# Optimization experiments

Measured on AMD Instinct MI355X. Metric: run time of the kernel, lower is better.

Reference implementation:

```python
import jax, jax.numpy as jnp
import numpy as np

RC = 6.0  # cosine cutoff radius

def _cut_fn(r):
    # Behler cosine cutoff: 0.5*(cos(pi*r/rc)+1) for r < rc, else 0
    return jnp.where(r < RC, 0.5 * (jnp.cos(jnp.pi * r / RC) + 1.0), 0.0)

def setup_inputs() -> dict:
    key = jax.random.key(0)
    ks = jax.random.split(key, 6)
    B, N, T, E, Z = 4, 256, 512, 16, 4
    def dist(k):
        return jax.random.uniform(k, (B, N, T), dtype=jnp.float32) * 5.0 + 0.5
    r_ij = dist(ks[0])
    r_ik = dist(ks[1])
    r_jk = dist(ks[2])
    # binary triple mask (float, as multiplied in the original forward)
    mask_triples = (jax.random.uniform(ks[3], (B, N, T)) > 0.3).astype(jnp.float32)
    etas = jax.random.uniform(ks[4], (E,), dtype=jnp.float32) + 0.5
    zetas = jnp.array([1.0, 2.0, 4.0, 8.0], dtype=jnp.float32)
    return {"r_ij": r_ij, "r_ik": r_ik, "r_jk": r_jk,
            "mask_triples": mask_triples, "etas": etas, "zetas": zetas}

def reference(r_ij, r_ik, r_jk, mask_triples, etas, zetas):
    # r_ij, r_ik, r_jk, mask_triples: (B, N, T); etas: (E,); zetas: (Z,)
    r2 = r_ij ** 2 + r_ik ** 2 + r_jk ** 2                       # (B,N,T)
    cut = _cut_fn(r_ij) * _cut_fn(r_ik) * _cut_fn(r_jk)          # (B,N,T)
    radius_part = jnp.exp(-r2[..., None] * etas) * cut[..., None]  # (B,N,T,E)
    cos_theta = r2 / (2.0 * r_ij * r_ik)                          # (B,N,T)
    cos_theta = jnp.where(mask_triples == 0, 0.0, cos_theta)
    base = (1.0 - cos_theta)[..., None] ** zetas                  # (B,N,T,Z)
    angular_part = jnp.concatenate(
        [2.0 ** (1.0 - zetas) * base, 2.0 ** (1.0 + zetas) * base], axis=-1
    )                                                             # (B,N,T,2Z)
    # fused masked outer-product + sum over triples dim (dim 2 in the original)
    f = jnp.einsum('bnt,bnte,bntz->bnez', mask_triples, radius_part, angular_part)
    B, N = r_ij.shape[:2]
    return f.reshape(B, N, -1)                                    # (B,N,E*2Z)
```

## Files before the change

kernel.cpp:

```cpp
#include <hip/hip_runtime.h>
#include <math.h>


#define T_TRIP 512
#define E_N 16

__global__ __launch_bounds__(256) void behler_g2_kernel(
    const float* __restrict__ r_ij, const float* __restrict__ r_ik,
    const float* __restrict__ r_jk, const float* __restrict__ mask,
    const float* __restrict__ etas, const float* __restrict__ zetas,
    float* __restrict__ out)
{
    __shared__ float  R2[T_TRIP];
    __shared__ float4 P[T_TRIP];
    __shared__ float  red[4][E_N][4];

    const int blk = blockIdx.x;
    const int tid = threadIdx.x;
    const size_t b2 = (size_t)blk * (T_TRIP / 2) + tid;

    const float z0 = zetas[0], z1 = zetas[1], z2 = zetas[2], z3 = zetas[3];
    const bool fastz = (z0 == 1.0f && z1 == 2.0f && z2 == 4.0f && z3 == 8.0f);
    const float PI_OVER_RC = 0.52359877559829887f;

    const float2 va = ((const float2*)r_ij)[b2];
    const float2 vb = ((const float2*)r_ik)[b2];
    const float2 vc = ((const float2*)r_jk)[b2];
    const float2 vm = ((const float2*)mask)[b2];

    float r2s[2];
    float4 ps[2];
    #pragma unroll
    for (int k = 0; k < 2; ++k) {
        float a = k ? va.y : va.x;
        float b = k ? vb.y : vb.x;
        float c = k ? vc.y : vc.x;
        float m = k ? vm.y : vm.x;
        float r2 = fmaf(a, a, fmaf(b, b, c * c));
        float fa  = (a < 6.0f) ? 0.5f * (__cosf(a * PI_OVER_RC) + 1.0f) : 0.0f;
        float fb  = (b < 6.0f) ? 0.5f * (__cosf(b * PI_OVER_RC) + 1.0f) : 0.0f;
        float fcv = (c < 6.0f) ? 0.5f * (__cosf(c * PI_OVER_RC) + 1.0f) : 0.0f;
        float w = m * fa * fb * fcv;
        float ct = __fdividef(r2, 2.0f * a * b);
        float4 p;
        if (fastz) {
            float bs = 1.0f - ct;
            float b2v = bs * bs, b4 = b2v * b2v, b8 = b4 * b4;
            p = make_float4(w * bs, w * b2v, w * b4, w * b8);
        } else {
            if (m == 0.0f) ct = 0.0f;
            float bs = 1.0f - ct;
            p = make_float4(w * powf(bs, z0), w * powf(bs, z1),
                            w * powf(bs, z2), w * powf(bs, z3));
        }
        r2s[k] = r2;
        ps[k] = p;
    }
    ((float2*)R2)[tid] = make_float2(r2s[0], r2s[1]);
    P[2 * tid]     = ps[0];
    P[2 * tid + 1] = ps[1];
    __syncthreads();

    const int g = tid >> 4;
    const int e = tid & 15;
    const float me = -etas[e];

    float acc0 = 0.0f, acc1 = 0.0f, acc2 = 0.0f, acc3 = 0.0f;
    #pragma unroll
    for (int i = 0; i < T_TRIP / 16; ++i) {
        int t = (i << 4) + g;
        float x = __expf(R2[t] * me);
        float4 p = P[t];
        acc0 = fmaf(x, p.x, acc0);
        acc1 = fmaf(x, p.y, acc1);
        acc2 = fmaf(x, p.z, acc2);
        acc3 = fmaf(x, p.w, acc3);
    }

    acc0 += __shfl_down(acc0, 32); acc0 += __shfl_down(acc0, 16);
    acc1 += __shfl_down(acc1, 32); acc1 += __shfl_down(acc1, 16);
    acc2 += __shfl_down(acc2, 32); acc2 += __shfl_down(acc2, 16);
    acc3 += __shfl_down(acc3, 32); acc3 += __shfl_down(acc3, 16);

    const int wave = tid >> 6;
    if ((tid & 63) < 16) {
        red[wave][e][0] = acc0;
        red[wave][e][1] = acc1;
        red[wave][e][2] = acc2;
        red[wave][e][3] = acc3;
    }
    __syncthreads();

    if (tid < 128) {
        int ee = tid >> 3, z = tid & 7, j = z & 3;
        float s = red[0][ee][j] + red[1][ee][j] + red[2][ee][j] + red[3][ee][j];
        float zj = zetas[j];
        float coef = exp2f((z < 4) ? (1.0f - zj) : (1.0f + zj));
        out[(size_t)blk * 128 + tid] = coef * s;
    }
}

extern "C" void kernel_launch(void* const* d_in, const int* in_sizes, int n_in,
                              void* d_out, int out_size, void* d_ws, size_t ws_size,
                              hipStream_t stream) {
    const float* r_ij = (const float*)d_in[0];
    const float* r_ik = (const float*)d_in[1];
    const float* r_jk = (const float*)d_in[2];
    const float* mask = (const float*)d_in[3];
    const float* etas = (const float*)d_in[4];
    const float* zetas = (const float*)d_in[5];
    float* out = (float*)d_out;

    int nblk = out_size / 128;
    behler_g2_kernel<<<nblk, 256, 0, stream>>>(r_ij, r_ik, r_jk, mask,
                                               etas, zetas, out);
}
```

Measured before the change: 9.734 us.

## Pack r2/base/log-weight in shared memory and fold weight into exp2

Instead of storing a float4 of weighted angular powers per triple, each triple now stores r2, the angular base and log2 of its cutoff weight in a repacked shared layout. In the main loop the weight is folded into the exponent via exp2(r2*eta*log2e + log2 w), and the zeta powers are recomputed by squaring in the inner loop. This reduces LDS traffic per triple at the cost of extra multiplies per (e, triple). A zero weight now relies on log2(0) giving -inf so that exp2 returns zero.

```diff
diff --git a/kernel.cpp b/kernel.cpp
--- a/kernel.cpp
+++ b/kernel.cpp
@@ -3,6 +3,7 @@
 
 
 #define T_TRIP 512
+#define NPAIR  (T_TRIP / 2)
 #define E_N 16
 
 __global__ __launch_bounds__(256) void behler_g2_kernel(
@@ -11,8 +12,8 @@
     const float* __restrict__ etas, const float* __restrict__ zetas,
     float* __restrict__ out)
 {
-    __shared__ float  R2[T_TRIP];
-    __shared__ float4 P[T_TRIP];
+    __shared__ float4 RB[NPAIR];
+    __shared__ float2 LW[NPAIR];
     __shared__ float  red[4][E_N][4];
 
     const int blk = blockIdx.x;
@@ -22,16 +23,16 @@
     const float z0 = zetas[0], z1 = zetas[1], z2 = zetas[2], z3 = zetas[3];
     const bool fastz = (z0 == 1.0f && z1 == 2.0f && z2 == 4.0f && z3 == 8.0f);
     const float PI_OVER_RC = 0.52359877559829887f;
+    const float LOG2E      = 1.4426950408889634f;
 
     const float2 va = ((const float2*)r_ij)[b2];
     const float2 vb = ((const float2*)r_ik)[b2];
     const float2 vc = ((const float2*)r_jk)[b2];
     const float2 vm = ((const float2*)mask)[b2];
 
-    float r2s[2];
-    float4 ps[2];
     #pragma unroll
     for (int k = 0; k < 2; ++k) {
+        int t = 2 * tid + k;
         float a = k ? va.y : va.x;
         float b = k ? vb.y : vb.x;
         float c = k ? vc.y : vc.x;
@@ -42,39 +43,52 @@
         float fcv = (c < 6.0f) ? 0.5f * (__cosf(c * PI_OVER_RC) + 1.0f) : 0.0f;
         float w = m * fa * fb * fcv;
         float ct = __fdividef(r2, 2.0f * a * b);
-        float4 p;
-        if (fastz) {
-            float bs = 1.0f - ct;
-            float b2v = bs * bs, b4 = b2v * b2v, b8 = b4 * b4;
-            p = make_float4(w * bs, w * b2v, w * b4, w * b8);
-        } else {
-            if (m == 0.0f) ct = 0.0f;
-            float bs = 1.0f - ct;
-            p = make_float4(w * powf(bs, z0), w * powf(bs, z1),
-                            w * powf(bs, z2), w * powf(bs, z3));
-        }
-        r2s[k] = r2;
-        ps[k] = p;
+        float bs = 1.0f - ct;
+        if (!fastz && m == 0.0f) bs = 0.0f;
+        float lw = __log2f(w);
+
+        int p    = (t >> 5) * 16 + (t & 15);
+        int slot = (t >> 4) & 1;
+        ((float2*)&RB[p])[slot] = make_float2(r2, bs);
+        ((float*)&LW[p])[slot]  = lw;
     }
-    ((float2*)R2)[tid] = make_float2(r2s[0], r2s[1]);
-    P[2 * tid]     = ps[0];
-    P[2 * tid + 1] = ps[1];
     __syncthreads();
 
     const int g = tid >> 4;
     const int e = tid & 15;
-    const float me = -etas[e];
+    const float me = -etas[e] * LOG2E;
 
     float acc0 = 0.0f, acc1 = 0.0f, acc2 = 0.0f, acc3 = 0.0f;
-    #pragma unroll
-    for (int i = 0; i < T_TRIP / 16; ++i) {
-        int t = (i << 4) + g;
-        float x = __expf(R2[t] * me);
-        float4 p = P[t];
-        acc0 = fmaf(x, p.x, acc0);
-        acc1 = fmaf(x, p.y, acc1);
-        acc2 = fmaf(x, p.z, acc2);
-        acc3 = fmaf(x, p.w, acc3);
+    if (fastz) {
+        #pragma unroll
+        for (int i = 0; i < NPAIR / 16; ++i) {
+            float4 rb = RB[i * 16 + g];
+            float2 lw = LW[i * 16 + g];
+            float xa = exp2f(fmaf(rb.x, me, lw.x));
+            float xb = exp2f(fmaf(rb.z, me, lw.y));
+            float s1 = rb.y, s2 = s1 * s1, s4 = s2 * s2, s8 = s4 * s4;
+            acc0 = fmaf(xa, s1, acc0);
+            acc1 = fmaf(xa, s2, acc1);
+            acc2 = fmaf(xa, s4, acc2);
+            acc3 = fmaf(xa, s8, acc3);
+            float u1 = rb.w, u2 = u1 * u1, u4 = u2 * u2, u8 = u4 * u4;
+            acc0 = fmaf(xb, u1, acc0);
+            acc1 = fmaf(xb, u2, acc1);
+            acc2 = fmaf(xb, u4, acc2);
+            acc3 = fmaf(xb, u8, acc3);
+        }
+    } else {
+        #pragma unroll 1
+        for (int i = 0; i < NPAIR / 16; ++i) {
+            float4 rb = RB[i * 16 + g];
+            float2 lw = LW[i * 16 + g];
+            float xa = exp2f(fmaf(rb.x, me, lw.x));
+            float xb = exp2f(fmaf(rb.z, me, lw.y));
+            acc0 = fmaf(xa, powf(rb.y, z0), acc0) + xb * powf(rb.w, z0);
+            acc1 = fmaf(xa, powf(rb.y, z1), acc1) + xb * powf(rb.w, z1);
+            acc2 = fmaf(xa, powf(rb.y, z2), acc2) + xb * powf(rb.w, z2);
+            acc3 = fmaf(xa, powf(rb.y, z3), acc3) + xb * powf(rb.w, z3);
+        }
     }
 
     acc0 += __shfl_down(acc0, 32); acc0 += __shfl_down(acc0, 16);
```

After: 10.47 us. 7.6% more time.
